# Performance work log

Hardware: AMD Instinct MI355X
Metric: run time of the kernel (lower is better)

## Reference

```python
import jax, jax.numpy as jnp
import numpy as np

B, D_IN, N, T = 128, 2048, 2048, 50
TAU_M = 4.0
BN_EPS = 1e-4
SIGMA = 0.4  # fixed sigma param of the erfc surrogate (requires_grad=False)


def setup_inputs() -> dict:
    key = jax.random.key(0)
    ks = jax.random.split(key, 4)
    input_spikes = jax.random.uniform(ks[0], (B, D_IN, T), dtype=jnp.float32)
    # Linear(input_size, neuron_number) with bias (train_bias=True)
    W = jax.random.normal(ks[1], (N, D_IN), dtype=jnp.float32) / np.sqrt(D_IN)
    b = jax.random.normal(ks[2], (N,), dtype=jnp.float32) * 0.01
    # per-timestep BN affine scale (bias removed: bntt_layer.bias = None)
    gamma = jnp.ones((T, N), dtype=jnp.float32)
    decay = np.exp(-1.0 / TAU_M).astype(np.float32)
    decay_v = jnp.full((N,), decay)
    reset_decay = jnp.full((N,), decay)
    reset_v = jnp.ones((N,), dtype=jnp.float32)
    return {"input_spikes": input_spikes, "W": W, "b": b, "gamma": gamma,
            "decay_v": decay_v, "reset_decay": reset_decay, "reset_v": reset_v}


def _spike(v):
    # erfc surrogate threshold: hard Heaviside at 1.0 in the forward pass
    return (v > 1.0).astype(v.dtype)


def reference(input_spikes, W, b, gamma, decay_v, reset_decay, reset_v):
    # input_spikes: [B, D_IN, T] -> time-major [T, B, D_IN]
    x_t = jnp.transpose(input_spikes, (2, 0, 1))

    def step(carry, xs):
        prev_v, prev_reset = carry            # [B, N] each
        x, g = xs                             # [B, D_IN], [N]
        psp = x @ W.T + b                     # [B, N]
        # BatchNorm1d in training mode: batch stats (biased var), no bias term
        mean = psp.mean(axis=0)
        var = psp.var(axis=0)
        bn = g * (psp - mean) * jax.lax.rsqrt(var + BN_EPS)
        cur_v = prev_v * decay_v + bn - prev_reset   # membrane_filter=True
        s = _spike(cur_v)
        cur_reset = prev_reset * reset_decay + s * reset_v
        return (cur_v, cur_reset), s

    init = (jnp.zeros((B, N), jnp.float32), jnp.zeros((B, N), jnp.float32))
    (final_v, final_reset), spikes = jax.lax.scan(step, init, (x_t, gamma))
    # spikes: [T, B, N] -> [B, N, T] (torch.stack(spikes, dim=-1))
    spikes = jnp.transpose(spikes, (1, 2, 0))
    return spikes, (final_v, final_reset)
```

## Files before the change

### kernel.cpp

```cpp
#include <hip/hip_runtime.h>
#include <cstddef>
#include <math.h>

#define BATCH 128
#define DIN   2048
#define NN    2048
#define TT    50
#define MM    (BATCH * TT)
#define BN_EPS 1e-4
#define NDIG  4

typedef double double4_t __attribute__((ext_vector_type(4)));
typedef int    int4v    __attribute__((ext_vector_type(4)));
typedef int    int16v   __attribute__((ext_vector_type(16)));

#define SWZ(x) (((x) & 7) << 2)


__device__ __forceinline__ void gload16(const void* g, void* l) {
    __builtin_amdgcn_global_load_lds(
        (const __attribute__((address_space(1))) void*)g,
        (__attribute__((address_space(3))) void*)l, 16, 0, 0);
}

__global__ __launch_bounds__(256) void split_a_kernel(
    const float* __restrict__ X,
    signed char* __restrict__ Adig)
{
    __shared__ float Xs[64 * TT];

    const int b  = blockIdx.x;
    const int gy = blockIdx.y;
    const int tid = threadIdx.x;
    const float* Xb = X + (size_t)b * (DIN * TT);

    for (int k0 = gy * (DIN / 8); k0 < (gy + 1) * (DIN / 8); k0 += 64) {
        for (int idx = tid; idx < 64 * TT; idx += 256)
            Xs[idx] = Xb[k0 * TT + idx];
        __syncthreads();
        for (int idx = tid; idx < 4 * TT; idx += 256) {
            const int t   = idx % TT;
            const int kg  = idx / TT;
            const int kl16 = kg << 4;
            const int mrow = b * TT + t;
            const int mp  = mrow >> 5;
            const int row = mrow & 31;
            const int kcl = (k0 + kl16) >> 5;
            const int sub = ((kl16 >> 4) & 1) << 9;

            signed char dig[NDIG][16];
#pragma unroll
            for (int j = 0; j < 16; ++j) {
                float r = Xs[(kl16 + j) * TT + t] * 64.f;
#pragma unroll
                for (int i = 0; i < NDIG; ++i) {
                    float di = rintf(r);
                    r = (r - di) * 128.f;
                    dig[i][j] = (signed char)(int)di;
                }
            }
#pragma unroll
            for (int i = 0; i < NDIG; ++i)
                *(int4*)&Adig[((((size_t)i * (MM / 32) + mp) * (DIN / 32) + kcl)
                               << 10) + sub + (row << 4)] = *(const int4*)dig[i];
        }
        __syncthreads();
    }
}

__global__ __launch_bounds__(256) void split_b_kernel(
    const float* __restrict__ W,
    signed char* __restrict__ Bdig,
    double* __restrict__ invB)
{
    __shared__ float red[256];
    __shared__ float sBsh;
    const int tid = threadIdx.x;
    for (int rep = 0; rep < 4; ++rep) {
        const int n = blockIdx.x * 4 + rep;
        const float* Wr = W + (size_t)n * DIN;
        float m_loc = 0.f;
        for (int k = tid; k < DIN; k += 256)
            m_loc = fmaxf(m_loc, fabsf(Wr[k]));
        red[tid] = m_loc;
        __syncthreads();
        for (int s = 128; s > 0; s >>= 1) {
            if (tid < s) red[tid] = fmaxf(red[tid], red[tid + s]);
            __syncthreads();
        }
        if (tid == 0) {
            float m = (red[0] == 0.f) ? 1.f : red[0];
            int ex; frexpf(m, &ex);
            sBsh = exp2f((float)(6 - ex));
            invB[n] = ldexp(1.0, ex - 6);
        }
        __syncthreads();
        const float sB = sBsh;
        const int np   = n >> 5;
        const int rowb = (n & 31) << 4;
        for (int g = tid; g < DIN / 16; g += 256) {
            const int k16 = g << 4;
            const int kc  = k16 >> 5;
            const int sub = ((k16 >> 4) & 1) << 9;
            signed char dig[NDIG][16];
#pragma unroll
            for (int j = 0; j < 16; ++j) {
                float r = Wr[k16 + j] * sB;
#pragma unroll
                for (int i = 0; i < NDIG; ++i) {
                    float di = rintf(r);
                    r = (r - di) * 128.f;
                    dig[i][j] = (signed char)(int)di;
                }
            }
#pragma unroll
            for (int i = 0; i < NDIG; ++i)
                *(int4*)&Bdig[((((size_t)i * (NN / 32) + np) * (DIN / 32) + kc)
                               << 10) + sub + rowb] = *(const int4*)dig[i];
        }
        __syncthreads();
    }
}

#define PAIRS(NH, BARR)                                                    \
    __builtin_amdgcn_s_setprio(1);                                         \
    _Pragma("unroll")                                                      \
    for (int kc = 0; kc < 2; ++kc)                                         \
        _Pragma("unroll")                                                  \
        for (int i = 0; i < NDIG; ++i)                                     \
            _Pragma("unroll")                                              \
            for (int j = 0; j + i < NDIG; ++j)                             \
                acc[NH][i + j] = __builtin_amdgcn_mfma_i32_32x32x32_i8(    \
                    a[kc][i], BARR[kc][j], acc[NH][i + j], 0, 0, 0);       \
    __builtin_amdgcn_s_setprio(0);

#define TILE(BUF, IT)                                                      \
    {                                                                      \
        int4v a[2][NDIG], bb[2][NDIG];                                     \
        _Pragma("unroll")                                                  \
        for (int c = 0; c < 2; ++c)                                        \
            _Pragma("unroll")                                              \
            for (int p = 0; p < NDIG; ++p) {                               \
                a[c][p]  = *(const int4v*)&Asd[BUF][p][wv][c][lane << 4];  \
                bb[c][p] = *(const int4v*)&Bsd[p][0][c][lane << 4];        \
            }                                                              \
        PAIRS(0, bb)                                                       \
        _Pragma("unroll")                                                  \
        for (int c = 0; c < 2; ++c)                                        \
            _Pragma("unroll")                                              \
            for (int p = 0; p < NDIG; ++p)                                 \
                bb[c][p] = *(const int4v*)&Bsd[p][1][c][lane << 4];        \
        __syncthreads();                                                   \
        if ((IT) + 1 < NIT) { stageA((BUF) ^ 1, (IT) + 1); stageB((IT) + 1); } \
        __builtin_amdgcn_sched_barrier(0);                                 \
        PAIRS(1, bb)                                                       \
        __syncthreads();                                                   \
    }

__global__ __launch_bounds__(256, 2) void gemm_i8_kernel(
    const signed char* __restrict__ Adig,
    const signed char* __restrict__ Bdig,
    const double* __restrict__ invB,
    float* __restrict__ PSP)
{
    __shared__ __align__(16) signed char Asd[2][NDIG][4][2][1024];
    __shared__ __align__(16) signed char Bsd[NDIG][2][2][1024];

    const int tid  = threadIdx.x;
    const int lane = tid & 63;
    const int wv   = tid >> 6;

    const int orig  = blockIdx.x;
    const int local = orig >> 3;
    const int n0 = (((orig & 7) << 2) + (local & 3)) << 6;
    const int m0 = (local >> 2) << 7;

    const int mpw = (m0 >> 5) + wv;
    const int np0 = n0 >> 5;
    const int bnh = wv & 1, bkc = wv >> 1;
    const size_t APL = ((size_t)(MM / 32) * (DIN / 32)) << 10;
    const size_t BPL = ((size_t)(NN / 32) * (DIN / 32)) << 10;
    const signed char* Abase =
        Adig + (((size_t)mpw * (DIN / 32)) << 10) + (lane << 4);
    const signed char* Bbase =
        Bdig + (((size_t)(np0 + bnh) * (DIN / 32)) << 10) + (lane << 4);

    auto stageA = [&](int buf, int kt) {
#pragma unroll
        for (int p = 0; p < NDIG; ++p)
#pragma unroll
            for (int c = 0; c < 2; ++c)
                gload16(Abase + (size_t)p * APL + ((size_t)((kt << 1) + c) << 10),
                        &Asd[buf][p][wv][c][0]);
    };
    auto stageB = [&](int kt) {
#pragma unroll
        for (int p = 0; p < NDIG; ++p)
            gload16(Bbase + (size_t)p * BPL + ((size_t)((kt << 1) + bkc) << 10),
                    &Bsd[p][bnh][bkc][0]);
    };

    int16v acc[2][NDIG];
#pragma unroll
    for (int nh = 0; nh < 2; ++nh)
#pragma unroll
        for (int w = 0; w < NDIG; ++w)
#pragma unroll
            for (int e = 0; e < 16; ++e) acc[nh][w][e] = 0;

    stageA(0, 0);
    stageB(0);
    __syncthreads();

    const int NIT = DIN / 64;
    for (int it = 0; it < NIT; it += 2) {
        TILE(0, it);
        TILE(1, it + 1);
    }

    const double c1 = 1.0 / 128.0, c2 = c1 * c1, c3 = c2 * c1;
    const double invA = 1.0 / 64.0;
    const int colr  = lane & 31;
    const int rbase = m0 + (wv << 5) + 4 * (lane >> 5);
#pragma unroll
    for (int nh = 0; nh < 2; ++nh) {
        const int ncol = n0 + (nh << 5) + colr;
        const double ib = invA * invB[ncol];
#pragma unroll
        for (int reg = 0; reg < 16; ++reg) {
            const int mrow = rbase + (reg & 3) + 8 * (reg >> 2);
            double s = (double)acc[nh][0][reg]
                     + c1 * (double)acc[nh][1][reg]
                     + c2 * (double)acc[nh][2][reg]
                     + c3 * (double)acc[nh][3][reg];
            PSP[(size_t)mrow * NN + ncol] = (float)(s * ib);
        }
    }
}

#define BKK 32

template <typename PT>
__global__ __launch_bounds__(256, 5) void gemm_psp_kernel(
    const float* __restrict__ X,
    const float* __restrict__ W,
    PT* __restrict__ PSP)
{
    __shared__ float As[2][BKK][64];
    __shared__ float Bs[2][64][BKK];

    const int tid = threadIdx.x;
    const int m0 = blockIdx.y * 64;
    const int n0 = blockIdx.x * 64;

    const int a_m = tid & 63;
    const int a_k = tid >> 6;
    const int m_g = m0 + a_m;
    const int ab  = m_g / TT;
    const int at  = m_g - ab * TT;
    const float* Aptr = X + (size_t)ab * (DIN * TT) + at;

    const int b_n = tid >> 2;
    const int b_k = (tid & 3) * 8;
    const float* Wptr = W + (size_t)(n0 + b_n) * DIN + b_k;
    const int bswz_st = SWZ(b_n);

    const int lane = tid & 63;
    const int wv   = tid >> 6;
    const int wm   = (wv >> 1) * 32;
    const int wn   = (wv & 1) * 32;
    const int row  = lane & 15;
    const int grp  = lane >> 4;
    const int bswz_rd = SWZ(row);

    double4_t acc[2][2];
#pragma unroll
    for (int i = 0; i < 2; ++i)
#pragma unroll
        for (int j = 0; j < 2; ++j) acc[i][j] = double4_t{0.0, 0.0, 0.0, 0.0};

    {
#pragma unroll
        for (int j = 0; j < 8; ++j) {
            const int kr = a_k + 4 * j;
            As[0][kr][a_m ^ SWZ(kr)] = Aptr[kr * TT];
        }
        *(float4*)&Bs[0][b_n][(b_k + 0) ^ bswz_st] = *(const float4*)(Wptr);
        *(float4*)&Bs[0][b_n][(b_k + 4) ^ bswz_st] = *(const float4*)(Wptr + 4);
    }

    const int NIT = DIN / BKK;
    for (int it = 0; it < NIT; ++it) {
        const int buf = it & 1;
        __syncthreads();

        float a_nxt[8];
        float4 b_nxt0, b_nxt1;
        if (it + 1 < NIT) {
            const int k0n = (it + 1) * BKK;
#pragma unroll
            for (int j = 0; j < 8; ++j)
                a_nxt[j] = Aptr[(k0n + a_k + 4 * j) * TT];
            b_nxt0 = *(const float4*)(Wptr + k0n);
            b_nxt1 = *(const float4*)(Wptr + k0n + 4);
        }

#pragma unroll
        for (int kq = 0; kq < BKK; kq += 4) {
            const int kr = kq + grp;
            const int aswz = SWZ(kr);
            const double a0 = (double)As[buf][kr][(wm + row) ^ aswz];
            const double a1 = (double)As[buf][kr][(wm + row + 16) ^ aswz];
            const double b0 = (double)Bs[buf][wn + row][kr ^ bswz_rd];
            const double b1 = (double)Bs[buf][wn + row + 16][kr ^ bswz_rd];
            acc[0][0] = __builtin_amdgcn_mfma_f64_16x16x4f64(a0, b0, acc[0][0], 0, 0, 0);
            acc[0][1] = __builtin_amdgcn_mfma_f64_16x16x4f64(a0, b1, acc[0][1], 0, 0, 0);
            acc[1][0] = __builtin_amdgcn_mfma_f64_16x16x4f64(a1, b0, acc[1][0], 0, 0, 0);
            acc[1][1] = __builtin_amdgcn_mfma_f64_16x16x4f64(a1, b1, acc[1][1], 0, 0, 0);
        }

        if (it + 1 < NIT) {
            const int nb = 1 - buf;
#pragma unroll
            for (int j = 0; j < 8; ++j) {
                const int kr = a_k + 4 * j;
                As[nb][kr][a_m ^ SWZ(kr)] = a_nxt[j];
            }
            *(float4*)&Bs[nb][b_n][(b_k + 0) ^ bswz_st] = b_nxt0;
            *(float4*)&Bs[nb][b_n][(b_k + 4) ^ bswz_st] = b_nxt1;
        }
    }

#pragma unroll
    for (int i = 0; i < 2; ++i)
#pragma unroll
        for (int j = 0; j < 2; ++j)
#pragma unroll
            for (int r = 0; r < 4; ++r) {
                const int mrow = m0 + wm + 16 * i + grp + 4 * r;
                PSP[(size_t)mrow * NN + (n0 + wn + 16 * j + row)] = (PT)acc[i][j][r];
            }
}

template <typename PT>
__global__ __launch_bounds__(256) void stats_kernel(
    const PT* __restrict__ PSP, const float* __restrict__ bias,
    double* __restrict__ mean_out, double* __restrict__ invstd_out)
{
    const int t = blockIdx.x >> 3;
    const int n = ((blockIdx.x & 7) << 8) + threadIdx.x;
    const double bb = (double)bias[n];
    const PT* p = PSP + (size_t)t * NN + n;

    double s = 0.0, ss = 0.0;
#pragma unroll 8
    for (int b = 0; b < BATCH; ++b) {
        const double v = (double)p[(size_t)b * (TT * NN)];
        s += v; ss += v * v;
    }
    const double mu0 = s * (1.0 / BATCH);
    const double var = fmax(ss * (1.0 / BATCH) - mu0 * mu0, 0.0);
    mean_out[t * NN + n]   = mu0 + bb;
    invstd_out[t * NN + n] = 1.0 / sqrt(var + BN_EPS);
}

template <typename PT>
__global__ __launch_bounds__(256) void recur_kernel(
    const PT* __restrict__ PSP, const float* __restrict__ bias,
    const double* __restrict__ mean_arr, const double* __restrict__ invstd_arr,
    const float* __restrict__ gamma, const float* __restrict__ decay_v,
    const float* __restrict__ reset_decay, const float* __restrict__ reset_v,
    float* __restrict__ out)
{
    __shared__ float spk[256 * (TT + 1)];

    const int b  = blockIdx.x >> 3;
    const int nc = blockIdx.x & 7;
    const int n  = (nc << 8) + threadIdx.x;
    const int tid = threadIdx.x;

    const double dv = (double)decay_v[n];
    const double rd = (double)reset_decay[n];
    const double rv = (double)reset_v[n];
    const double bb = (double)bias[n];

    double v = 0.0, r = 0.0;
    const PT* p = PSP + (size_t)b * (TT * NN) + n;
    const float* ga = gamma + n;
    const double* me = mean_arr + n;
    const double* is = invstd_arr + n;

    for (int t = 0; t < TT; ++t) {
        const double psp = (double)p[t * NN] + bb;
        const double bn  = (double)ga[t * NN] * (psp - me[t * NN]) * is[t * NN];
        v = v * dv + bn - r;
        const double s = (v > 1.0) ? 1.0 : 0.0;
        r = r * rd + s * rv;
        spk[tid * (TT + 1) + t] = (float)s;
    }
    __syncthreads();

    const size_t base = (size_t)b * (NN * TT) + (size_t)nc * (256 * TT);
    for (int i = tid; i < 256 * TT; i += 256) {
        const int n_l = i / TT;
        out[base + i] = spk[n_l * (TT + 1) + (i - n_l * TT)];
    }

    const size_t fin = (size_t)BATCH * NN * TT;
    out[fin + (size_t)b * NN + n]                      = (float)v;
    out[fin + (size_t)BATCH * NN + (size_t)b * NN + n] = (float)r;
}

template <typename PT>
static void launch_fp64(const float* X, const float* W, const float* bias,
                        const float* gamma, const float* decay_v,
                        const float* reset_dec, const float* reset_v,
                        float* out, void* d_ws, hipStream_t stream)
{
    PT* PSP = (PT*)d_ws;
    char* after = (char*)d_ws + (size_t)MM * NN * sizeof(PT);
    double* meanA  = (double*)after;
    double* invstd = meanA + (size_t)TT * NN;

    dim3 ggrid(NN / 64, MM / 64);
    gemm_psp_kernel<PT><<<ggrid, 256, 0, stream>>>(X, W, PSP);
    stats_kernel<PT><<<TT * (NN / 256), 256, 0, stream>>>(PSP, bias, meanA, invstd);
    recur_kernel<PT><<<BATCH * (NN / 256), 256, 0, stream>>>(
        PSP, bias, meanA, invstd, gamma, decay_v, reset_dec, reset_v, out);
}

extern "C" void kernel_launch(void* const* d_in, const int* in_sizes, int n_in,
                              void* d_out, int out_size, void* d_ws, size_t ws_size,
                              hipStream_t stream) {
    (void)in_sizes; (void)n_in; (void)out_size;
    const float* X          = (const float*)d_in[0];
    const float* W          = (const float*)d_in[1];
    const float* bias       = (const float*)d_in[2];
    const float* gamma      = (const float*)d_in[3];
    const float* decay_v    = (const float*)d_in[4];
    const float* reset_dec  = (const float*)d_in[5];
    const float* reset_v    = (const float*)d_in[6];
    float* out = (float*)d_out;

    const size_t psp_f   = (size_t)MM * NN * sizeof(float);
    const size_t psp_d   = (size_t)MM * NN * sizeof(double);
    const size_t stats_b = (size_t)TT * NN * 2 * sizeof(double);
    const size_t adig_b  = (size_t)NDIG * MM * DIN;
    const size_t bdig_b  = (size_t)NDIG * NN * DIN;
    const size_t need_i8 = psp_f + stats_b + adig_b + bdig_b + NN * sizeof(double);
    const size_t need_d  = psp_d + stats_b;

    if (ws_size >= need_i8) {
        float*  PSP    = (float*)d_ws;
        char*   cur    = (char*)d_ws + psp_f;
        double* meanA  = (double*)cur;              cur += (size_t)TT * NN * 8;
        double* invstd = (double*)cur;              cur += (size_t)TT * NN * 8;
        signed char* Adig = (signed char*)cur;      cur += adig_b;
        signed char* Bdig = (signed char*)cur;      cur += bdig_b;
        double* invB   = (double*)cur;

        split_a_kernel<<<dim3(BATCH, 8), 256, 0, stream>>>(X, Adig);
        split_b_kernel<<<NN / 4, 256, 0, stream>>>(W, Bdig, invB);
        gemm_i8_kernel<<<dim3((MM / 128) * (NN / 64)), 256, 0, stream>>>(
            Adig, Bdig, invB, PSP);
        stats_kernel<float><<<TT * (NN / 256), 256, 0, stream>>>(PSP, bias, meanA, invstd);
        recur_kernel<float><<<BATCH * (NN / 256), 256, 0, stream>>>(
            PSP, bias, meanA, invstd, gamma, decay_v, reset_dec, reset_v, out);
    } else if (ws_size >= need_d) {
        launch_fp64<double>(X, W, bias, gamma, decay_v, reset_dec, reset_v, out, d_ws, stream);
    } else {
        launch_fp64<float>(X, W, bias, gamma, decay_v, reset_dec, reset_v, out, d_ws, stream);
    }
}
```

Measured before the change: 460.3 us.

## Merge digit-split kernels and make int8 GEMM a persistent tile-loop grid

The two kernels that split X and W into int8 digits become one launch, with blocks branching by index, which saves one launch and lets the two jobs overlap. The int8 GEMM now launches 512 persistent blocks that loop over the 1600 output tiles, keeping the XCD-aware n-tile mapping. This targets launch overhead and tail effects. In exchange, each block carries a variable number of tiles, and the loop adds some bookkeeping.

```diff
diff --git a/kernel.cpp b/kernel.cpp
--- a/kernel.cpp
+++ b/kernel.cpp
@@ -23,102 +23,104 @@
         (__attribute__((address_space(3))) void*)l, 16, 0, 0);
 }
 
-__global__ __launch_bounds__(256) void split_a_kernel(
+__global__ __launch_bounds__(256) void split_ab_kernel(
     const float* __restrict__ X,
-    signed char* __restrict__ Adig)
-{
-    __shared__ float Xs[64 * TT];
-
-    const int b  = blockIdx.x;
-    const int gy = blockIdx.y;
-    const int tid = threadIdx.x;
-    const float* Xb = X + (size_t)b * (DIN * TT);
-
-    for (int k0 = gy * (DIN / 8); k0 < (gy + 1) * (DIN / 8); k0 += 64) {
-        for (int idx = tid; idx < 64 * TT; idx += 256)
-            Xs[idx] = Xb[k0 * TT + idx];
-        __syncthreads();
-        for (int idx = tid; idx < 4 * TT; idx += 256) {
-            const int t   = idx % TT;
-            const int kg  = idx / TT;
-            const int kl16 = kg << 4;
-            const int mrow = b * TT + t;
-            const int mp  = mrow >> 5;
-            const int row = mrow & 31;
-            const int kcl = (k0 + kl16) >> 5;
-            const int sub = ((kl16 >> 4) & 1) << 9;
-
-            signed char dig[NDIG][16];
-#pragma unroll
-            for (int j = 0; j < 16; ++j) {
-                float r = Xs[(kl16 + j) * TT + t] * 64.f;
-#pragma unroll
-                for (int i = 0; i < NDIG; ++i) {
-                    float di = rintf(r);
-                    r = (r - di) * 128.f;
-                    dig[i][j] = (signed char)(int)di;
-                }
-            }
-#pragma unroll
-            for (int i = 0; i < NDIG; ++i)
-                *(int4*)&Adig[((((size_t)i * (MM / 32) + mp) * (DIN / 32) + kcl)
-                               << 10) + sub + (row << 4)] = *(const int4*)dig[i];
-        }
-        __syncthreads();
-    }
-}
-
-__global__ __launch_bounds__(256) void split_b_kernel(
     const float* __restrict__ W,
+    signed char* __restrict__ Adig,
     signed char* __restrict__ Bdig,
     double* __restrict__ invB)
 {
+    __shared__ float Xs[64 * TT];
     __shared__ float red[256];
     __shared__ float sBsh;
+
     const int tid = threadIdx.x;
-    for (int rep = 0; rep < 4; ++rep) {
-        const int n = blockIdx.x * 4 + rep;
-        const float* Wr = W + (size_t)n * DIN;
-        float m_loc = 0.f;
-        for (int k = tid; k < DIN; k += 256)
-            m_loc = fmaxf(m_loc, fabsf(Wr[k]));
-        red[tid] = m_loc;
-        __syncthreads();
-        for (int s = 128; s > 0; s >>= 1) {
-            if (tid < s) red[tid] = fmaxf(red[tid], red[tid + s]);
+
+    if (blockIdx.x < 1024) {
+        const int b  = blockIdx.x >> 3;
+        const int gy = blockIdx.x & 7;
+        const float* Xb = X + (size_t)b * (DIN * TT);
+
+        for (int k0 = gy * (DIN / 8); k0 < (gy + 1) * (DIN / 8); k0 += 64) {
+            for (int idx = tid; idx < 64 * TT; idx += 256)
+                Xs[idx] = Xb[k0 * TT + idx];
             __syncthreads();
-        }
-        if (tid == 0) {
-            float m = (red[0] == 0.f) ? 1.f : red[0];
-            int ex; frexpf(m, &ex);
-            sBsh = exp2f((float)(6 - ex));
-            invB[n] = ldexp(1.0, ex - 6);
-        }
-        __syncthreads();
-        const float sB = sBsh;
-        const int np   = n >> 5;
-        const int rowb = (n & 31) << 4;
-        for (int g = tid; g < DIN / 16; g += 256) {
-            const int k16 = g << 4;
-            const int kc  = k16 >> 5;
-            const int sub = ((k16 >> 4) & 1) << 9;
-            signed char dig[NDIG][16];
-#pragma unroll
-            for (int j = 0; j < 16; ++j) {
-                float r = Wr[k16 + j] * sB;
-#pragma unroll
-                for (int i = 0; i < NDIG; ++i) {
-                    float di = rintf(r);
-                    r = (r - di) * 128.f;
-                    dig[i][j] = (signed char)(int)di;
+            for (int idx = tid; idx < 4 * TT; idx += 256) {
+                const int t    = idx % TT;
+                const int kg   = idx / TT;
+                const int kl16 = kg << 4;
+                const int mrow = b * TT + t;
+                const int mp   = mrow >> 5;
+                const int row  = mrow & 31;
+                const int kcl  = (k0 + kl16) >> 5;
+                const int sub  = ((kl16 >> 4) & 1) << 9;
+
+                signed char dig[NDIG][16];
+#pragma unroll
+                for (int j = 0; j < 16; ++j) {
+                    float r = Xs[(kl16 + j) * TT + t] * 64.f;
+#pragma unroll
+                    for (int i = 0; i < NDIG; ++i) {
+                        float di = rintf(r);
+                        r = (r - di) * 128.f;
+                        dig[i][j] = (signed char)(int)di;
+                    }
                 }
-            }
-#pragma unroll
-            for (int i = 0; i < NDIG; ++i)
-                *(int4*)&Bdig[((((size_t)i * (NN / 32) + np) * (DIN / 32) + kc)
-                               << 10) + sub + rowb] = *(const int4*)dig[i];
-        }
-        __syncthreads();
+#pragma unroll
+                for (int i = 0; i < NDIG; ++i)
+                    *(int4*)&Adig[((((size_t)i * (MM / 32) + mp) * (DIN / 32)
+                                    + kcl) << 10) + sub + (row << 4)]
+                        = *(const int4*)dig[i];
+            }
+            __syncthreads();
+        }
+    } else {
+        const int nb = blockIdx.x - 1024;
+        for (int rep = 0; rep < 4; ++rep) {
+            const int n = nb * 4 + rep;
+            const float* Wr = W + (size_t)n * DIN;
+            float m_loc = 0.f;
+            for (int k = tid; k < DIN; k += 256)
+                m_loc = fmaxf(m_loc, fabsf(Wr[k]));
+            red[tid] = m_loc;
+            __syncthreads();
+            for (int s = 128; s > 0; s >>= 1) {
+                if (tid < s) red[tid] = fmaxf(red[tid], red[tid + s]);
+                __syncthreads();
+            }
+            if (tid == 0) {
+                float m = (red[0] == 0.f) ? 1.f : red[0];
+                int ex; frexpf(m, &ex);
+                sBsh = exp2f((float)(6 - ex));
+                invB[n] = ldexp(1.0, ex - 6);
+            }
+            __syncthreads();
+            const float sB = sBsh;
+            const int np   = n >> 5;
+            const int rowb = (n & 31) << 4;
+            for (int g = tid; g < DIN / 16; g += 256) {
+                const int k16 = g << 4;
+                const int kc  = k16 >> 5;
+                const int sub = ((k16 >> 4) & 1) << 9;
+                signed char dig[NDIG][16];
+#pragma unroll
+                for (int j = 0; j < 16; ++j) {
+                    float r = Wr[k16 + j] * sB;
+#pragma unroll
+                    for (int i = 0; i < NDIG; ++i) {
+                        float di = rintf(r);
+                        r = (r - di) * 128.f;
+                        dig[i][j] = (signed char)(int)di;
+                    }
+                }
+#pragma unroll
+                for (int i = 0; i < NDIG; ++i)
+                    *(int4*)&Bdig[((((size_t)i * (NN / 32) + np) * (DIN / 32)
+                                    + kc) << 10) + sub + rowb]
+                        = *(const int4*)dig[i];
+            }
+            __syncthreads();
+        }
     }
 }
 
@@ -170,70 +172,75 @@
     const int lane = tid & 63;
     const int wv   = tid >> 6;
 
-    const int orig  = blockIdx.x;
-    const int local = orig >> 3;
-    const int n0 = (((orig & 7) << 2) + (local & 3)) << 6;
-    const int m0 = (local >> 2) << 7;
-
-    const int mpw = (m0 >> 5) + wv;
-    const int np0 = n0 >> 5;
+    const int xcd  = blockIdx.x & 7;
+    const int slot = blockIdx.x >> 3;
+
     const int bnh = wv & 1, bkc = wv >> 1;
     const size_t APL = ((size_t)(MM / 32) * (DIN / 32)) << 10;
     const size_t BPL = ((size_t)(NN / 32) * (DIN / 32)) << 10;
-    const signed char* Abase =
-        Adig + (((size_t)mpw * (DIN / 32)) << 10) + (lane << 4);
-    const signed char* Bbase =
-        Bdig + (((size_t)(np0 + bnh) * (DIN / 32)) << 10) + (lane << 4);
-
-    auto stageA = [&](int buf, int kt) {
-#pragma unroll
-        for (int p = 0; p < NDIG; ++p)
-#pragma unroll
-            for (int c = 0; c < 2; ++c)
-                gload16(Abase + (size_t)p * APL + ((size_t)((kt << 1) + c) << 10),
-                        &Asd[buf][p][wv][c][0]);
-    };
-    auto stageB = [&](int kt) {
-#pragma unroll
-        for (int p = 0; p < NDIG; ++p)
-            gload16(Bbase + (size_t)p * BPL + ((size_t)((kt << 1) + bkc) << 10),
-                    &Bsd[p][bnh][bkc][0]);
-    };
-
-    int16v acc[2][NDIG];
-#pragma unroll
-    for (int nh = 0; nh < 2; ++nh)
-#pragma unroll
-        for (int w = 0; w < NDIG; ++w)
-#pragma unroll
-            for (int e = 0; e < 16; ++e) acc[nh][w][e] = 0;
-
-    stageA(0, 0);
-    stageB(0);
-    __syncthreads();
-
     const int NIT = DIN / 64;
-    for (int it = 0; it < NIT; it += 2) {
-        TILE(0, it);
-        TILE(1, it + 1);
-    }
-
-    const double c1 = 1.0 / 128.0, c2 = c1 * c1, c3 = c2 * c1;
-    const double invA = 1.0 / 64.0;
-    const int colr  = lane & 31;
-    const int rbase = m0 + (wv << 5) + 4 * (lane >> 5);
-#pragma unroll
-    for (int nh = 0; nh < 2; ++nh) {
-        const int ncol = n0 + (nh << 5) + colr;
-        const double ib = invA * invB[ncol];
-#pragma unroll
-        for (int reg = 0; reg < 16; ++reg) {
-            const int mrow = rbase + (reg & 3) + 8 * (reg >> 2);
-            double s = (double)acc[nh][0][reg]
-                     + c1 * (double)acc[nh][1][reg]
-                     + c2 * (double)acc[nh][2][reg]
-                     + c3 * (double)acc[nh][3][reg];
-            PSP[(size_t)mrow * NN + ncol] = (float)(s * ib);
+
+    for (int ti = slot; ti < 200; ti += 64) {
+        const int n0 = ((xcd << 2) + (ti & 3)) << 6;
+        const int m0 = (ti >> 2) << 7;
+
+        const int mpw = (m0 >> 5) + wv;
+        const signed char* Abase =
+            Adig + (((size_t)mpw * (DIN / 32)) << 10) + (lane << 4);
+        const signed char* Bbase =
+            Bdig + (((size_t)((n0 >> 5) + bnh) * (DIN / 32)) << 10) + (lane << 4);
+
+        auto stageA = [&](int buf, int kt) {
+#pragma unroll
+            for (int p = 0; p < NDIG; ++p)
+#pragma unroll
+                for (int c = 0; c < 2; ++c)
+                    gload16(Abase + (size_t)p * APL
+                                  + ((size_t)((kt << 1) + c) << 10),
+                            &Asd[buf][p][wv][c][0]);
+        };
+        auto stageB = [&](int kt) {
+#pragma unroll
+            for (int p = 0; p < NDIG; ++p)
+                gload16(Bbase + (size_t)p * BPL
+                              + ((size_t)((kt << 1) + bkc) << 10),
+                        &Bsd[p][bnh][bkc][0]);
+        };
+
+        int16v acc[2][NDIG];
+#pragma unroll
+        for (int nh = 0; nh < 2; ++nh)
+#pragma unroll
+            for (int w = 0; w < NDIG; ++w)
+#pragma unroll
+                for (int e = 0; e < 16; ++e) acc[nh][w][e] = 0;
+
+        stageA(0, 0);
+        stageB(0);
+        __syncthreads();
+
+        for (int it = 0; it < NIT; it += 2) {
+            TILE(0, it);
+            TILE(1, it + 1);
+        }
+
+        const double c1 = 1.0 / 128.0, c2 = c1 * c1, c3 = c2 * c1;
+        const double invA = 1.0 / 64.0;
+        const int colr  = lane & 31;
+        const int rbase = m0 + (wv << 5) + 4 * (lane >> 5);
+#pragma unroll
+        for (int nh = 0; nh < 2; ++nh) {
+            const int ncol = n0 + (nh << 5) + colr;
+            const double ib = invA * invB[ncol];
+#pragma unroll
+            for (int reg = 0; reg < 16; ++reg) {
+                const int mrow = rbase + (reg & 3) + 8 * (reg >> 2);
+                double s = (double)acc[nh][0][reg]
+                         + c1 * (double)acc[nh][1][reg]
+                         + c2 * (double)acc[nh][2][reg]
+                         + c3 * (double)acc[nh][3][reg];
+                PSP[(size_t)mrow * NN + ncol] = (float)(s * ib);
+            }
         }
     }
 }
@@ -459,10 +466,8 @@
         signed char* Bdig = (signed char*)cur;      cur += bdig_b;
         double* invB   = (double*)cur;
 
-        split_a_kernel<<<dim3(BATCH, 8), 256, 0, stream>>>(X, Adig);
-        split_b_kernel<<<NN / 4, 256, 0, stream>>>(W, Bdig, invB);
-        gemm_i8_kernel<<<dim3((MM / 128) * (NN / 64)), 256, 0, stream>>>(
-            Adig, Bdig, invB, PSP);
+        split_ab_kernel<<<1536, 256, 0, stream>>>(X, W, Adig, Bdig, invB);
+        gemm_i8_kernel<<<512, 256, 0, stream>>>(Adig, Bdig, invB, PSP);
         stats_kernel<float><<<TT * (NN / 256), 256, 0, stream>>>(PSP, bias, meanA, invstd);
         recur_kernel<float><<<BATCH * (NN / 256), 256, 0, stream>>>(
             PSP, bias, meanA, invstd, gamma, decay_v, reset_dec, reset_v, out);
```

Measured after the change: 442.8 us, median of 2. -3.8%, faster.
